# Performance work log

Hardware: AMD Instinct MI355X
Metric: run time of the kernel (lower is better)

Reference implementation:

```python
import jax, jax.numpy as jnp
import numpy as np

T, B = 1024, 16384

def setup_inputs() -> dict:
    key = jax.random.key(0)
    ks = jax.random.split(key, 8)
    return {
        "inputs": jax.random.normal(ks[0], (T, B, 6), dtype=jnp.float32),
        "targets": jax.random.normal(ks[1], (T, B, 1), dtype=jnp.float32),
        "Wx": jax.random.normal(ks[2], (6, 6), dtype=jnp.float32) * 0.3,
        "Wu": jax.random.normal(ks[3], (6, 1), dtype=jnp.float32) * 0.3,
        "W1": jax.random.normal(ks[4], (20, 12), dtype=jnp.float32) * 0.3,
        "b1": jax.random.normal(ks[5], (20,), dtype=jnp.float32) * 0.1,
        "W2": jax.random.normal(ks[6], (1, 20), dtype=jnp.float32) * 0.3,
        "b2": jax.random.normal(ks[7], (1,), dtype=jnp.float32) * 0.1,
        "epoch": 10,
        "maxepoch": 100,
        "forceswitch": 2,
    }

def reference(inputs, targets, Wx, Wu, W1, b1, W2, b2, epoch, maxepoch, forceswitch):
    # forceswitch == 2 => deterministic teacher forcing: the feedback `output`
    # at step k is targets[k-1] for k > 0 and zeros at k = 0.
    assert forceswitch == 2
    Tlen, Bsz, _ = inputs.shape
    prev_out = jnp.concatenate(
        [jnp.zeros((1, Bsz, 1), dtype=inputs.dtype), targets[:-1]], axis=0
    )  # [T, B, 1]

    def step(db, xs):
        x_k, u_k = xs  # [B, 6], [B, 1]
        db = db @ Wx.T + u_k @ Wu.T                 # delay buffer update [B, 6]
        ni = jnp.concatenate([db, x_k], axis=-1)    # [B, 12]
        h = jnp.tanh(ni @ W1.T + b1)                # [B, 20]
        out = h @ W2.T + b2                         # [B, 1]
        return db, out

    db0 = jnp.zeros((Bsz, 6), dtype=inputs.dtype)
    _, outputs = jax.lax.scan(step, db0, (inputs, prev_out))
    return outputs  # [T, B, 1]
```

## Files before the change

### kernel.cpp

```cpp
#include <hip/hip_runtime.h>
#include <cstddef>

#define TT 1024
#define BB 16384
#define LC 32
#define CC (TT / LC)

__device__ __forceinline__ float pade_tanh(float x) {
    float cx = fminf(fmaxf(x, -4.97f), 4.97f);
    float s  = cx * cx;
    float n  = cx * fmaf(s, fmaf(s, (s + 378.0f), 17325.0f), 135135.0f);
    float d  = fmaf(s, fmaf(s, fmaf(s, 28.0f, 3150.0f), 62370.0f), 135135.0f);
    return n * __builtin_amdgcn_rcpf(d);
}

__global__ __launch_bounds__(256) void k_phase1(
    const float* __restrict__ targets,
    const float* __restrict__ Wx,
    const float* __restrict__ Wu,
    float* __restrict__ v)
{
    const int b = blockIdx.x * 256 + threadIdx.x;
    const int c = blockIdx.y;
    float wx[6][6], wu[6];
#pragma unroll
    for (int i = 0; i < 6; ++i) {
        wu[i] = Wu[i];
#pragma unroll
        for (int j = 0; j < 6; ++j) wx[i][j] = Wx[i * 6 + j];
    }
    float db[6] = {0.f, 0.f, 0.f, 0.f, 0.f, 0.f};
    const int t0 = c * LC;
#pragma unroll 4
    for (int s = 0; s < LC; ++s) {
        const int t = t0 + s;
        float u = 0.0f;
        if (t > 0) u = targets[(size_t)(t - 1) * BB + b];
        float nd[6];
#pragma unroll
        for (int i = 0; i < 6; ++i) {
            float a = u * wu[i];
#pragma unroll
            for (int j = 0; j < 6; ++j) a = fmaf(db[j], wx[i][j], a);
            nd[i] = a;
        }
#pragma unroll
        for (int i = 0; i < 6; ++i) db[i] = nd[i];
    }
#pragma unroll
    for (int i = 0; i < 6; ++i) v[((size_t)c * 6 + i) * BB + b] = db[i];
}

__global__ __launch_bounds__(256) void k_phase2(
    const float* __restrict__ Wx,
    float* __restrict__ v)
{
    const int b = blockIdx.x * 256 + threadIdx.x;
    float M[6][6];
#pragma unroll
    for (int i = 0; i < 6; ++i)
#pragma unroll
        for (int j = 0; j < 6; ++j)
            M[j][i] = Wx[i * 6 + j];
    for (int it = 0; it < 5; ++it) {
        float P[6][6];
#pragma unroll
        for (int i = 0; i < 6; ++i)
#pragma unroll
            for (int j = 0; j < 6; ++j) {
                float a = 0.0f;
#pragma unroll
                for (int k = 0; k < 6; ++k) a = fmaf(M[i][k], M[k][j], a);
                P[i][j] = a;
            }
#pragma unroll
        for (int i = 0; i < 6; ++i)
#pragma unroll
            for (int j = 0; j < 6; ++j) M[i][j] = P[i][j];
    }
    float db[6] = {0.f, 0.f, 0.f, 0.f, 0.f, 0.f};
    for (int c = 0; c < CC; ++c) {
        float vv[6];
#pragma unroll
        for (int i = 0; i < 6; ++i) {
            const size_t idx = ((size_t)c * 6 + i) * BB + b;
            vv[i] = v[idx];
            v[idx] = db[i];
        }
        float nd[6];
#pragma unroll
        for (int i = 0; i < 6; ++i) {
            float a = vv[i];
#pragma unroll
            for (int j = 0; j < 6; ++j) a = fmaf(db[j], M[j][i], a);
            nd[i] = a;
        }
#pragma unroll
        for (int i = 0; i < 6; ++i) db[i] = nd[i];
    }
}

__global__ __launch_bounds__(256, 2) void k_phase3(
    const float* __restrict__ inputs,
    const float* __restrict__ targets,
    const float* __restrict__ Wxg,
    const float* __restrict__ Wug,
    const float* __restrict__ W1g,
    const float* __restrict__ b1g,
    const float* __restrict__ W2g,
    const float* __restrict__ b2g,
    const float* __restrict__ dbs,
    float* __restrict__ out)
{
    const int tid  = threadIdx.x;
    const int half = tid & 1;
    const int b    = blockIdx.x * 128 + (tid >> 1);
    const int c    = blockIdx.y;
    const int m0   = half * 10;

    float wx[6][6], wu[6];
#pragma unroll
    for (int i = 0; i < 6; ++i) {
        wu[i] = Wug[i];
#pragma unroll
        for (int j = 0; j < 6; ++j) wx[i][j] = Wxg[i * 6 + j];
    }
    const float vb2 = b2g[0];

    float2 w1p[5][12];
    float2 vb1[5], vw2[5];
#pragma unroll
    for (int p = 0; p < 5; ++p) {
        const int ma = m0 + p, mb = m0 + p + 5;
#pragma unroll
        for (int j = 0; j < 12; ++j) {
            w1p[p][j].x = W1g[ma * 12 + j];
            w1p[p][j].y = W1g[mb * 12 + j];
        }
        vb1[p].x = b1g[ma]; vb1[p].y = b1g[mb];
        vw2[p].x = W2g[ma]; vw2[p].y = W2g[mb];
    }

    float db[6];
#pragma unroll
    for (int i = 0; i < 6; ++i) db[i] = dbs[((size_t)c * 6 + i) * BB + b];

    const int t0 = c * LC;
    float u_cur = (t0 == 0) ? 0.0f : targets[(size_t)(t0 - 1) * BB + b];
    const float2* xp = reinterpret_cast<const float2*>(inputs + ((size_t)t0 * BB + b) * 6);
    float2 x0 = xp[0], x1 = xp[1], x2 = xp[2];

    for (int s = 0; s < LC; ++s) {
        const int t = t0 + s;
        float u_nxt = 0.0f;
        float2 n0 = x0, n1 = x1, n2 = x2;
        if (s + 1 < LC) {
            u_nxt = targets[(size_t)t * BB + b];
            const float2* xpn =
                reinterpret_cast<const float2*>(inputs + ((size_t)(t + 1) * BB + b) * 6);
            n0 = xpn[0]; n1 = xpn[1]; n2 = xpn[2];
        }

        float nd[6];
#pragma unroll
        for (int i = 0; i < 6; ++i) {
            float a = u_cur * wu[i];
#pragma unroll
            for (int j = 0; j < 6; ++j) a = fmaf(db[j], wx[i][j], a);
            nd[i] = a;
        }
#pragma unroll
        for (int i = 0; i < 6; ++i) db[i] = nd[i];

        const float ni[12] = {db[0], db[1], db[2], db[3], db[4], db[5],
                              x0.x, x0.y, x1.x, x1.y, x2.x, x2.y};

        float2 acc[5];
#pragma unroll
        for (int p = 0; p < 5; ++p) acc[p] = vb1[p];
#pragma unroll
        for (int j = 0; j < 12; ++j) {
            const float nij = ni[j];
#pragma unroll
            for (int p = 0; p < 5; ++p) {
                acc[p].x = fmaf(w1p[p][j].x, nij, acc[p].x);
                acc[p].y = fmaf(w1p[p][j].y, nij, acc[p].y);
            }
        }

        float2 osum = {0.0f, 0.0f};
#pragma unroll
        for (int p = 0; p < 5; ++p) {
            float tx = pade_tanh(acc[p].x);
            float ty = pade_tanh(acc[p].y);
            osum.x = fmaf(vw2[p].x, tx, osum.x);
            osum.y = fmaf(vw2[p].y, ty, osum.y);
        }
        float oh = osum.x + osum.y;
        float o  = oh + __shfl_xor(oh, 1, 64) + vb2;
        if (half == 0) out[(size_t)t * BB + b] = o;

        u_cur = u_nxt; x0 = n0; x1 = n1; x2 = n2;
    }
}

extern "C" void kernel_launch(void* const* d_in, const int* in_sizes, int n_in,
                              void* d_out, int out_size, void* d_ws, size_t ws_size,
                              hipStream_t stream) {
    (void)in_sizes; (void)n_in; (void)out_size; (void)ws_size;
    const float* inputs  = (const float*)d_in[0];
    const float* targets = (const float*)d_in[1];
    const float* Wx = (const float*)d_in[2];
    const float* Wu = (const float*)d_in[3];
    const float* W1 = (const float*)d_in[4];
    const float* b1 = (const float*)d_in[5];
    const float* W2 = (const float*)d_in[6];
    const float* b2 = (const float*)d_in[7];
    float* out = (float*)d_out;
    float* v   = (float*)d_ws;

    dim3 blk(256);
    dim3 g1(BB / 256, CC);
    hipLaunchKernelGGL(k_phase1, g1, blk, 0, stream, targets, Wx, Wu, v);
    hipLaunchKernelGGL(k_phase2, dim3(BB / 256), blk, 0, stream, Wx, v);
    dim3 g3(BB / 128, CC);
    hipLaunchKernelGGL(k_phase3, g3, blk, 0, stream,
                       inputs, targets, Wx, Wu, W1, b1, W2, b2, v, out);
}
```

Measured before the change: 821.5 us.

## Process two batch columns per thread with packed FP32 math and exp-based tanh

Each thread pair in phase 3 now handles two adjacent batch columns, packed into 2-wide vectors so the compiler can emit packed FMA instructions for the delay-buffer update and the hidden layer. The Pade tanh approximation is replaced by an exp2/reciprocal formulation. Inputs, targets and outputs are loaded and stored as wider vectors, and the grid in x is halved to match. This aims to cut per-element instruction count and raise memory access width, at the cost of more registers per thread and changed tanh numerics.

```diff
diff --git a/kernel.cpp b/kernel.cpp
--- a/kernel.cpp
+++ b/kernel.cpp
@@ -6,12 +6,24 @@
 #define LC 32
 #define CC (TT / LC)
 
-__device__ __forceinline__ float pade_tanh(float x) {
-    float cx = fminf(fmaxf(x, -4.97f), 4.97f);
-    float s  = cx * cx;
-    float n  = cx * fmaf(s, fmaf(s, (s + 378.0f), 17325.0f), 135135.0f);
-    float d  = fmaf(s, fmaf(s, fmaf(s, 28.0f, 3150.0f), 62370.0f), 135135.0f);
-    return n * __builtin_amdgcn_rcpf(d);
+typedef float v2f __attribute__((ext_vector_type(2)));
+
+__device__ __forceinline__ v2f splat2(float x) { v2f r; r.x = x; r.y = x; return r; }
+
+#if __has_builtin(__builtin_amdgcn_exp2f)
+#define EXP2F(x) __builtin_amdgcn_exp2f(x)
+#else
+#define EXP2F(x) __expf((x) * 0.6931471805599453f)
+#endif
+
+__device__ __forceinline__ v2f tanh2(v2f x) {
+    v2f y = x * 2.885390081777927f;
+    float ex = EXP2F(y.x);
+    float ey = EXP2F(y.y);
+    v2f r;
+    r.x = __builtin_amdgcn_rcpf(ex + 1.0f);
+    r.y = __builtin_amdgcn_rcpf(ey + 1.0f);
+    return __builtin_elementwise_fma(splat2(-2.0f), r, splat2(1.0f));
 }
 
 __global__ __launch_bounds__(256) void k_phase1(
@@ -114,7 +126,8 @@
 {
     const int tid  = threadIdx.x;
     const int half = tid & 1;
-    const int b    = blockIdx.x * 128 + (tid >> 1);
+    const int pair = tid >> 1;
+    const int col  = blockIdx.x * 256 + pair * 2;
     const int c    = blockIdx.y;
     const int m0   = half * 10;
 
@@ -127,80 +140,85 @@
     }
     const float vb2 = b2g[0];
 
-    float2 w1p[5][12];
-    float2 vb1[5], vw2[5];
-#pragma unroll
-    for (int p = 0; p < 5; ++p) {
-        const int ma = m0 + p, mb = m0 + p + 5;
-#pragma unroll
-        for (int j = 0; j < 12; ++j) {
-            w1p[p][j].x = W1g[ma * 12 + j];
-            w1p[p][j].y = W1g[mb * 12 + j];
-        }
-        vb1[p].x = b1g[ma]; vb1[p].y = b1g[mb];
-        vw2[p].x = W2g[ma]; vw2[p].y = W2g[mb];
-    }
-
-    float db[6];
-#pragma unroll
-    for (int i = 0; i < 6; ++i) db[i] = dbs[((size_t)c * 6 + i) * BB + b];
+    float w1[10][12], vb1[10], vw2[10];
+#pragma unroll
+    for (int m = 0; m < 10; ++m) {
+#pragma unroll
+        for (int j = 0; j < 12; ++j) w1[m][j] = W1g[(m0 + m) * 12 + j];
+        vb1[m] = b1g[m0 + m];
+        vw2[m] = W2g[m0 + m];
+    }
+
+    v2f db[6];
+#pragma unroll
+    for (int i = 0; i < 6; ++i)
+        db[i] = *(const v2f*)&dbs[((size_t)c * 6 + i) * BB + col];
 
     const int t0 = c * LC;
-    float u_cur = (t0 == 0) ? 0.0f : targets[(size_t)(t0 - 1) * BB + b];
-    const float2* xp = reinterpret_cast<const float2*>(inputs + ((size_t)t0 * BB + b) * 6);
-    float2 x0 = xp[0], x1 = xp[1], x2 = xp[2];
+    v2f u_cur = splat2(0.0f);
+    if (t0 > 0) u_cur = *(const v2f*)&targets[(size_t)(t0 - 1) * BB + col];
+    const float4* xp = (const float4*)(inputs + ((size_t)t0 * BB + col) * 6);
+    float4 a0 = xp[0], a1 = xp[1], a2 = xp[2];
 
     for (int s = 0; s < LC; ++s) {
         const int t = t0 + s;
-        float u_nxt = 0.0f;
-        float2 n0 = x0, n1 = x1, n2 = x2;
+        v2f u_nxt = splat2(0.0f);
+        float4 p0 = a0, p1 = a1, p2 = a2;
         if (s + 1 < LC) {
-            u_nxt = targets[(size_t)t * BB + b];
-            const float2* xpn =
-                reinterpret_cast<const float2*>(inputs + ((size_t)(t + 1) * BB + b) * 6);
-            n0 = xpn[0]; n1 = xpn[1]; n2 = xpn[2];
-        }
-
-        float nd[6];
-#pragma unroll
-        for (int i = 0; i < 6; ++i) {
-            float a = u_cur * wu[i];
-#pragma unroll
-            for (int j = 0; j < 6; ++j) a = fmaf(db[j], wx[i][j], a);
+            u_nxt = *(const v2f*)&targets[(size_t)t * BB + col];
+            const float4* xpn =
+                (const float4*)(inputs + ((size_t)(t + 1) * BB + col) * 6);
+            p0 = xpn[0]; p1 = xpn[1]; p2 = xpn[2];
+        }
+
+        v2f nd[6];
+#pragma unroll
+        for (int i = 0; i < 6; ++i) {
+            v2f a = u_cur * wu[i];
+#pragma unroll
+            for (int j = 0; j < 6; ++j)
+                a = __builtin_elementwise_fma(db[j], splat2(wx[i][j]), a);
             nd[i] = a;
         }
 #pragma unroll
         for (int i = 0; i < 6; ++i) db[i] = nd[i];
 
-        const float ni[12] = {db[0], db[1], db[2], db[3], db[4], db[5],
-                              x0.x, x0.y, x1.x, x1.y, x2.x, x2.y};
-
-        float2 acc[5];
-#pragma unroll
-        for (int p = 0; p < 5; ++p) acc[p] = vb1[p];
+        v2f ni[12];
+#pragma unroll
+        for (int i = 0; i < 6; ++i) ni[i] = db[i];
+        ni[6].x  = a0.x; ni[6].y  = a1.z;
+        ni[7].x  = a0.y; ni[7].y  = a1.w;
+        ni[8].x  = a0.z; ni[8].y  = a2.x;
+        ni[9].x  = a0.w; ni[9].y  = a2.y;
+        ni[10].x = a1.x; ni[10].y = a2.z;
+        ni[11].x = a1.y; ni[11].y = a2.w;
+
+        v2f acc[10];
+#pragma unroll
+        for (int m = 0; m < 10; ++m) acc[m] = splat2(vb1[m]);
 #pragma unroll
         for (int j = 0; j < 12; ++j) {
-            const float nij = ni[j];
-#pragma unroll
-            for (int p = 0; p < 5; ++p) {
-                acc[p].x = fmaf(w1p[p][j].x, nij, acc[p].x);
-                acc[p].y = fmaf(w1p[p][j].y, nij, acc[p].y);
-            }
-        }
-
-        float2 osum = {0.0f, 0.0f};
-#pragma unroll
-        for (int p = 0; p < 5; ++p) {
-            float tx = pade_tanh(acc[p].x);
-            float ty = pade_tanh(acc[p].y);
-            osum.x = fmaf(vw2[p].x, tx, osum.x);
-            osum.y = fmaf(vw2[p].y, ty, osum.y);
-        }
-        float oh = osum.x + osum.y;
-        float o  = oh + __shfl_xor(oh, 1, 64) + vb2;
-        if (half == 0) out[(size_t)t * BB + b] = o;
-
-        u_cur = u_nxt; x0 = n0; x1 = n1; x2 = n2;
+            const v2f nij = ni[j];
+#pragma unroll
+            for (int m = 0; m < 10; ++m)
+                acc[m] = __builtin_elementwise_fma(splat2(w1[m][j]), nij, acc[m]);
+        }
+
+        v2f osum = splat2(0.0f);
+#pragma unroll
+        for (int m = 0; m < 10; ++m)
+            osum = __builtin_elementwise_fma(splat2(vw2[m]), tanh2(acc[m]), osum);
+
+        v2f other;
+        other.x = __shfl_xor(osum.x, 1, 64);
+        other.y = __shfl_xor(osum.y, 1, 64);
+        v2f o = osum + other + splat2(vb2);
+        if (half == 0) {
+            float2 st; st.x = o.x; st.y = o.y;
+            *(float2*)&out[(size_t)t * BB + col] = st;
+        }
+
+        u_cur = u_nxt; a0 = p0; a1 = p1; a2 = p2;
     }
 }
 
@@ -223,7 +241,7 @@
     dim3 g1(BB / 256, CC);
     hipLaunchKernelGGL(k_phase1, g1, blk, 0, stream, targets, Wx, Wu, v);
     hipLaunchKernelGGL(k_phase2, dim3(BB / 256), blk, 0, stream, Wx, v);
-    dim3 g3(BB / 128, CC);
+    dim3 g3(BB / 256, CC);
     hipLaunchKernelGGL(k_phase3, g3, blk, 0, stream,
                        inputs, targets, Wx, Wu, W1, b1, W2, b2, v, out);
 }
```

Measured after the change: 1.948 ms. +137.1%, slower.
